# Optimization experiments

Measured on AMD Instinct MI355X. Metric: run time of the kernel, lower is better.

## Reference

```python
import jax, jax.numpy as jnp
import numpy as np

B, T, DIM, HEADS, KPROJ = 4, 4096, 1024, 16, 256
DH = DIM // HEADS  # dim_head = 64


def setup_inputs() -> dict:
    key = jax.random.key(0)
    k1, k2, k3, k4 = jax.random.split(key, 4)
    x = jax.random.normal(k1, (B, T, DIM), dtype=jnp.float32)
    proj_mat = jax.random.normal(k2, (T, KPROJ), dtype=jnp.float32)
    # to_qvk: Linear(dim, 3*dim, bias=False); store as [dim, 3*dim] so y = x @ Wqkv
    Wqkv = jax.random.normal(k3, (DIM, 3 * DIM), dtype=jnp.float32) / np.sqrt(DIM)
    # W_0: Linear(dim, dim, bias=False); stored as [dim, dim] so y = x @ W0
    W0 = jax.random.normal(k4, (DIM, DIM), dtype=jnp.float32) / np.sqrt(DIM)
    return {"x": x, "proj_mat": proj_mat, "Wqkv": Wqkv, "W0": W0}


def reference(x, proj_mat, Wqkv, W0):
    scale = DH ** (-0.5)
    qkv = jnp.einsum('btc,cf->btf', x, Wqkv)  # [B,T,3*dim]
    # einops 'b t (d k h) -> k b h t d' with k=3, h=HEADS: last axis splits as (d, 3, h)
    qkv = qkv.reshape(B, T, DH, 3, HEADS)
    qkv = jnp.transpose(qkv, (3, 0, 4, 1, 2))  # [3, B, H, T, DH]
    q, k, v = qkv[0], qkv[1], qkv[2]
    # Linformer low-rank projection of k and v along sequence axis
    k = jnp.einsum('bhjd,jk->bhkd', k, proj_mat)  # [B,H,KPROJ,DH]
    v = jnp.einsum('bhjd,jk->bhkd', v, proj_mat)
    # scaled dot-product attention
    scores = jnp.einsum('bhid,bhjd->bhij', q, k) * scale  # [B,H,T,KPROJ]
    attn = jax.nn.softmax(scores, axis=-1)
    out = jnp.einsum('bhij,bhjd->bhid', attn, v)  # [B,H,T,DH]
    out = jnp.transpose(out, (0, 2, 1, 3)).reshape(B, T, HEADS * DH)
    return jnp.einsum('btc,cf->btf', out, W0)
```

## Files before the change

### kernel.cpp

```cpp
#include <hip/hip_runtime.h>
#include <stdint.h>
#include <stddef.h>

#define TB    4096
#define NDIM  1024
#define NH    16
#define KPROJ 256
#define DH    64
#define NBH   64

typedef _Float16 f16;
typedef _Float16 f16x8 __attribute__((ext_vector_type(8)));
typedef float    f32x4 __attribute__((ext_vector_type(4)));

__device__ __forceinline__ void glds16(const f16* g, f16* l) {
  __builtin_amdgcn_global_load_lds((const __attribute__((address_space(1))) void*)g,
                                   (__attribute__((address_space(3))) void*)l, 16, 0, 0);
}

__launch_bounds__(256)
__global__ void cvt_x(const float* __restrict__ in, f16* __restrict__ out) {
  size_t i = ((size_t)blockIdx.x * 256 + threadIdx.x) * 8;
  float4 v0 = *(const float4*)(in + i);
  float4 v1 = *(const float4*)(in + i + 4);
  union { f16 h[8]; uint4 u; } pk;
  pk.h[0] = (f16)v0.x; pk.h[1] = (f16)v0.y; pk.h[2] = (f16)v0.z; pk.h[3] = (f16)v0.w;
  pk.h[4] = (f16)v1.x; pk.h[5] = (f16)v1.y; pk.h[6] = (f16)v1.z; pk.h[7] = (f16)v1.w;
  *(uint4*)(out + i) = pk.u;
}

__launch_bounds__(256)
__global__ void cvt_t(const float* __restrict__ in, f16* __restrict__ out, int R, int C) {
  __shared__ __align__(16) f16 s[64][72];
  const int tid = threadIdx.x;
  const int c0 = blockIdx.x * 64, r0 = blockIdx.y * 64;
#pragma unroll
  for (int it = 0; it < 4; ++it) {
    int chunk = it * 256 + tid;
    int r_l = chunk >> 4, c4 = (chunk & 15) * 4;
    float4 v = *(const float4*)(in + (size_t)(r0 + r_l) * C + c0 + c4);
    s[c4 + 0][r_l] = (f16)v.x; s[c4 + 1][r_l] = (f16)v.y;
    s[c4 + 2][r_l] = (f16)v.z; s[c4 + 3][r_l] = (f16)v.w;
  }
  __syncthreads();
#pragma unroll
  for (int it = 0; it < 2; ++it) {
    int chunk = it * 256 + tid;
    int c_l = chunk >> 3, rc = (chunk & 7) * 8;
    *(uint4*)(out + (size_t)(c0 + c_l) * R + r0 + rc) = *(const uint4*)&s[c_l][rc];
  }
}

__launch_bounds__(256)
__global__ void k_qkv(const f16* __restrict__ Xh, const f16* __restrict__ Wt,
                      f16* __restrict__ qt, f16* __restrict__ kvt) {
  __shared__ __align__(16) f16 As[128 * 32];
  __shared__ __align__(16) f16 Bs[128 * 32];
  const int tid = threadIdx.x;
  const int w = tid >> 6, lane = tid & 63;
  const int quad = lane >> 4, l15 = lane & 15;
  const int bn0 = blockIdx.x * 128, bm0 = blockIdx.y * 128;
  const int wm = (w & 1) * 64, wn = (w >> 1) * 64;
  const int srow = lane >> 2, skc = lane & 3;

  f32x4 acc[4][4];
#pragma unroll
  for (int i = 0; i < 4; ++i)
#pragma unroll
    for (int j = 0; j < 4; ++j) acc[i][j] = (f32x4){0.f, 0.f, 0.f, 0.f};

  const f16* Ag0 = Xh + (size_t)(bm0 + w * 32 + srow) * NDIM + skc * 8;
  const f16* Bg0 = Wt + (size_t)(bn0 + w * 32 + srow) * NDIM + skc * 8;
  f16* Al0 = As + (w * 32) * 32;
  f16* Bl0 = Bs + (w * 32) * 32;

  for (int k0 = 0; k0 < NDIM; k0 += 32) {
    glds16(Ag0 + k0, Al0);
    glds16(Ag0 + (size_t)16 * NDIM + k0, Al0 + 16 * 32);
    glds16(Bg0 + k0, Bl0);
    glds16(Bg0 + (size_t)16 * NDIM + k0, Bl0 + 16 * 32);
    __syncthreads();
    f16x8 a[4], b[4];
#pragma unroll
    for (int i = 0; i < 4; ++i) a[i] = *(const f16x8*)(As + (wm + i * 16 + l15) * 32 + quad * 8);
#pragma unroll
    for (int j = 0; j < 4; ++j) b[j] = *(const f16x8*)(Bs + (wn + j * 16 + l15) * 32 + quad * 8);
#pragma unroll
    for (int i = 0; i < 4; ++i)
#pragma unroll
      for (int j = 0; j < 4; ++j)
        acc[i][j] = __builtin_amdgcn_mfma_f32_16x16x32_f16(a[i], b[j], acc[i][j], 0, 0, 0);
    __syncthreads();
  }

#pragma unroll
  for (int i = 0; i < 4; ++i) {
    int mrow = bm0 + wm + i * 16 + quad * 4;
    int bb = mrow >> 12, t = mrow & 4095;
#pragma unroll
    for (int j = 0; j < 4; ++j) {
      int f = bn0 + wn + j * 16 + l15;
      int d = f / 48;
      int rem = f - d * 48;
      int rr = rem >> 4, h = rem & 15;
      f16* base = (rr == 0) ? qt : kvt + (size_t)(rr - 1) * ((size_t)NBH * DH * TB);
      size_t off = ((size_t)((bb * NH + h) * DH + d)) * TB + t;
      union { f16 hh[4]; uint2 u; } pk;
#pragma unroll
      for (int r = 0; r < 4; ++r) pk.hh[r] = (f16)acc[i][j][r];
      *(uint2*)(base + off) = pk.u;
    }
  }
}

__launch_bounds__(256)
__global__ void k_proj(const f16* __restrict__ Pt, const f16* __restrict__ kvt,
                       f16* __restrict__ kpv) {
  __shared__ __align__(16) f16 As[128 * 32];
  __shared__ __align__(16) f16 Bs[64 * 32];
  const int tid = threadIdx.x;
  const int w = tid >> 6, lane = tid & 63;
  const int quad = lane >> 4, l15 = lane & 15;
  const int km0 = blockIdx.x * 128;
  const int bh = blockIdx.y, rv = blockIdx.z;
  const int srow = lane >> 2, skc = lane & 3;
  const f16* Bbase = kvt + (size_t)(rv * NBH + bh) * DH * TB;

  f32x4 acc[2][4];
#pragma unroll
  for (int i = 0; i < 2; ++i)
#pragma unroll
    for (int j = 0; j < 4; ++j) acc[i][j] = (f32x4){0.f, 0.f, 0.f, 0.f};

  const f16* Ag0 = Pt + (size_t)(km0 + w * 32 + srow) * TB + skc * 8;
  const f16* Bg0 = Bbase + (size_t)(w * 16 + srow) * TB + skc * 8;
  f16* Al0 = As + (w * 32) * 32;
  f16* Bl0 = Bs + (w * 16) * 32;

  for (int k0 = 0; k0 < TB; k0 += 32) {
    glds16(Ag0 + k0, Al0);
    glds16(Ag0 + (size_t)16 * TB + k0, Al0 + 16 * 32);
    glds16(Bg0 + k0, Bl0);
    __syncthreads();
    f16x8 a[2], b[4];
#pragma unroll
    for (int i = 0; i < 2; ++i) a[i] = *(const f16x8*)(As + (w * 32 + i * 16 + l15) * 32 + quad * 8);
#pragma unroll
    for (int j = 0; j < 4; ++j) b[j] = *(const f16x8*)(Bs + (j * 16 + l15) * 32 + quad * 8);
#pragma unroll
    for (int i = 0; i < 2; ++i)
#pragma unroll
      for (int j = 0; j < 4; ++j)
        acc[i][j] = __builtin_amdgcn_mfma_f32_16x16x32_f16(a[i], b[j], acc[i][j], 0, 0, 0);
    __syncthreads();
  }

  if (rv == 0) {
#pragma unroll
    for (int i = 0; i < 2; ++i) {
      int kap0 = km0 + w * 32 + i * 16 + quad * 4;
#pragma unroll
      for (int j = 0; j < 4; ++j) {
        int d = j * 16 + l15;
#pragma unroll
        for (int r = 0; r < 4; ++r)
          kpv[((size_t)bh * KPROJ + kap0 + r) * DH + d] = (f16)acc[i][j][r];
      }
    }
  } else {
    f16* vpT = kpv + (size_t)NBH * KPROJ * DH;
#pragma unroll
    for (int i = 0; i < 2; ++i) {
      int kap0 = km0 + w * 32 + i * 16 + quad * 4;
#pragma unroll
      for (int j = 0; j < 4; ++j) {
        int d = j * 16 + l15;
        union { f16 hh[4]; uint2 u; } pk;
#pragma unroll
        for (int r = 0; r < 4; ++r) pk.hh[r] = (f16)acc[i][j][r];
        *(uint2*)&vpT[((size_t)bh * DH + d) * KPROJ + kap0] = pk.u;
      }
    }
  }
}

__launch_bounds__(256)
__global__ void k_attn(const f16* __restrict__ qt, const f16* __restrict__ kpv,
                       f16* __restrict__ aout) {
  __shared__ __align__(16) f16 Ps[4][16][264];
  __shared__ __align__(16) f16 Ks[16384];
  f16* Qs = &Ps[0][0][0];
  const int tid = threadIdx.x;
  const int w = tid >> 6, lane = tid & 63;
  const int quad = lane >> 4, l15 = lane & 15;
  const int bh = blockIdx.y;
  const int tb = blockIdx.x * 64;
  const int b = bh >> 4, h = bh & 15;

  const f16* kpb = kpv + (size_t)bh * (KPROJ * DH);
  const f16* vpb = kpv + (size_t)NBH * KPROJ * DH + (size_t)bh * (DH * KPROJ);

  {
    const f16* qg = qt + (size_t)bh * DH * TB + tb;
#pragma unroll
    for (int c = 0; c < 2; ++c) {
      int d0 = w * 16 + c * 8;
      glds16(qg + (size_t)(d0 + (lane >> 3)) * TB + (lane & 7) * 8, Qs + d0 * 64);
    }
    const int kcolg = ((lane & 7) ^ (lane >> 3)) * 8;
    const int krow0 = w * 64 + (lane >> 3);
#pragma unroll
    for (int it = 0; it < 8; ++it)
      glds16(kpb + (size_t)(krow0 + it * 8) * DH + kcolg, Ks + w * 4096 + it * 512);
  }
  __syncthreads();

  f16x8 aq[2];
#pragma unroll
  for (int ks = 0; ks < 2; ++ks)
#pragma unroll
    for (int j = 0; j < 8; ++j)
      aq[ks][j] = Qs[(ks * 32 + quad * 8 + j) * 64 + w * 16 + l15];

  f32x4 sc[16];
  const int sc0 = (quad ^ (l15 & 7)) * 8;
#pragma unroll
  for (int nt = 0; nt < 16; ++nt) {
    const f16* krow = Ks + (nt * 16 + l15) * 64;
    f16x8 b0 = *(const f16x8*)(krow + sc0);
    f16x8 b1 = *(const f16x8*)(krow + (sc0 ^ 32));
    f32x4 c = (f32x4){0.f, 0.f, 0.f, 0.f};
    c = __builtin_amdgcn_mfma_f32_16x16x32_f16(aq[0], b0, c, 0, 0, 0);
    c = __builtin_amdgcn_mfma_f32_16x16x32_f16(aq[1], b1, c, 0, 0, 0);
    sc[nt] = c;
  }

  float mx[4] = {-1e30f, -1e30f, -1e30f, -1e30f};
#pragma unroll
  for (int nt = 0; nt < 16; ++nt)
#pragma unroll
    for (int r = 0; r < 4; ++r) {
      float s = sc[nt][r] * 0.125f;
      sc[nt][r] = s;
      mx[r] = fmaxf(mx[r], s);
    }
#pragma unroll
  for (int r = 0; r < 4; ++r)
#pragma unroll
    for (int off = 1; off < 16; off <<= 1) mx[r] = fmaxf(mx[r], __shfl_xor(mx[r], off));

  __syncthreads();

  {
#pragma unroll
    for (int it = 0; it < 8; ++it) {
      int r = w * 16 + it * 2 + (lane >> 5);
      int colg = ((lane & 31) ^ (r & 7)) * 8;
      glds16(vpb + (size_t)r * KPROJ + colg, Ks + w * 4096 + it * 512);
    }
  }

  float sm[4] = {0.f, 0.f, 0.f, 0.f};
#pragma unroll
  for (int nt = 0; nt < 16; ++nt)
#pragma unroll
    for (int r = 0; r < 4; ++r) {
      float e = __expf(sc[nt][r] - mx[r]);
      sc[nt][r] = e;
      sm[r] += e;
    }
#pragma unroll
  for (int r = 0; r < 4; ++r)
#pragma unroll
    for (int off = 1; off < 16; off <<= 1) sm[r] += __shfl_xor(sm[r], off);

#pragma unroll
  for (int nt = 0; nt < 16; ++nt)
#pragma unroll
    for (int r = 0; r < 4; ++r) {
      f16 hh = (f16)sc[nt][r];
      uint32_t hb = (uint32_t)__builtin_bit_cast(uint16_t, hh);
      uint32_t nb = (uint32_t)__shfl_xor((int)hb, 1);
      if (!(lane & 1))
        *(uint32_t*)&Ps[w][quad * 4 + r][nt * 16 + l15] = (hb & 0xffffu) | (nb << 16);
    }

  __syncthreads();

  f32x4 oc[4];
#pragma unroll
  for (int j = 0; j < 4; ++j) oc[j] = (f32x4){0.f, 0.f, 0.f, 0.f};
#pragma unroll
  for (int kk = 0; kk < 8; ++kk) {
    f16x8 pa = *(const f16x8*)&Ps[w][l15][kk * 32 + quad * 8];
#pragma unroll
    for (int nd = 0; nd < 4; ++nd) {
      int row = nd * 16 + l15;
      int c = ((kk * 4 + quad) ^ (l15 & 7)) * 8;
      f16x8 bv = *(const f16x8*)(Ks + row * KPROJ + c);
      oc[nd] = __builtin_amdgcn_mfma_f32_16x16x32_f16(pa, bv, oc[nd], 0, 0, 0);
    }
  }

#pragma unroll
  for (int nd = 0; nd < 4; ++nd)
#pragma unroll
    for (int r = 0; r < 4; ++r)
      Ps[w][quad * 4 + r][nd * 16 + l15] = (f16)(oc[nd][r] / sm[r]);

  const int orow = lane >> 3, oc8 = (lane & 7) * 8;
  const size_t obase = ((size_t)b * TB + tb + w * 16) * NDIM + h * 64 + oc8;
#pragma unroll
  for (int g = 0; g < 2; ++g)
    *(f16x8*)(aout + obase + (size_t)(g * 8 + orow) * NDIM) =
        *(const f16x8*)&Ps[w][g * 8 + orow][oc8];
}

__launch_bounds__(256)
__global__ void k_out(const f16* __restrict__ A, const f16* __restrict__ Bt,
                      float* __restrict__ Out) {
  __shared__ __align__(16) f16 As[128 * 32];
  __shared__ __align__(16) f16 Bs[128 * 32];
  const int tid = threadIdx.x;
  const int w = tid >> 6, lane = tid & 63;
  const int quad = lane >> 4, l15 = lane & 15;
  const int bn0 = blockIdx.x * 128, bm0 = blockIdx.y * 128;
  const int wm = (w & 1) * 64, wn = (w >> 1) * 64;
  const int srow = lane >> 2, skc = lane & 3;

  f32x4 acc[4][4];
#pragma unroll
  for (int i = 0; i < 4; ++i)
#pragma unroll
    for (int j = 0; j < 4; ++j) acc[i][j] = (f32x4){0.f, 0.f, 0.f, 0.f};

  const f16* Ag0 = A + (size_t)(bm0 + w * 32 + srow) * NDIM + skc * 8;
  const f16* Bg0 = Bt + (size_t)(bn0 + w * 32 + srow) * NDIM + skc * 8;
  f16* Al0 = As + (w * 32) * 32;
  f16* Bl0 = Bs + (w * 32) * 32;

  for (int k0 = 0; k0 < NDIM; k0 += 32) {
    glds16(Ag0 + k0, Al0);
    glds16(Ag0 + (size_t)16 * NDIM + k0, Al0 + 16 * 32);
    glds16(Bg0 + k0, Bl0);
    glds16(Bg0 + (size_t)16 * NDIM + k0, Bl0 + 16 * 32);
    __syncthreads();
    f16x8 a[4], b[4];
#pragma unroll
    for (int i = 0; i < 4; ++i) a[i] = *(const f16x8*)(As + (wm + i * 16 + l15) * 32 + quad * 8);
#pragma unroll
    for (int j = 0; j < 4; ++j) b[j] = *(const f16x8*)(Bs + (wn + j * 16 + l15) * 32 + quad * 8);
#pragma unroll
    for (int i = 0; i < 4; ++i)
#pragma unroll
      for (int j = 0; j < 4; ++j)
        acc[i][j] = __builtin_amdgcn_mfma_f32_16x16x32_f16(a[i], b[j], acc[i][j], 0, 0, 0);
    __syncthreads();
  }

#pragma unroll
  for (int i = 0; i < 4; ++i) {
    int m = bm0 + wm + i * 16 + quad * 4;
#pragma unroll
    for (int j = 0; j < 4; ++j) {
      int n = bn0 + wn + j * 16 + l15;
#pragma unroll
      for (int r = 0; r < 4; ++r) Out[(size_t)(m + r) * NDIM + n] = acc[i][j][r];
    }
  }
}

extern "C" void kernel_launch(void* const* d_in, const int* in_sizes, int n_in,
                              void* d_out, int out_size, void* d_ws, size_t ws_size,
                              hipStream_t stream) {
  const float* X    = (const float*)d_in[0];
  const float* P    = (const float*)d_in[1];
  const float* Wqkv = (const float*)d_in[2];
  const float* W0   = (const float*)d_in[3];
  float* Out = (float*)d_out;

  char* ws = (char*)d_ws;
  const size_t MB = 1ull << 20;
  f16* Xh   = (f16*)(ws);
  f16* aout = (f16*)(ws);
  f16* qt   = (f16*)(ws + 32 * MB);
  f16* kvt  = (f16*)(ws + 64 * MB);
  f16* kpv  = (f16*)(ws + 128 * MB);
  f16* Wqt  = (f16*)(ws + 132 * MB);
  f16* W0t  = (f16*)(ws + 138 * MB);
  f16* Ptb  = (f16*)(ws + 140 * MB);

  cvt_x<<<dim3(8192), 256, 0, stream>>>(X, Xh);
  cvt_t<<<dim3(48, 16), 256, 0, stream>>>(Wqkv, Wqt, 1024, 3072);
  cvt_t<<<dim3(16, 16), 256, 0, stream>>>(W0, W0t, 1024, 1024);
  cvt_t<<<dim3(4, 64), 256, 0, stream>>>(P, Ptb, 4096, 256);
  k_qkv<<<dim3(24, 128), 256, 0, stream>>>(Xh, Wqt, qt, kvt);
  k_proj<<<dim3(2, 64, 2), 256, 0, stream>>>(Ptb, kvt, kpv);
  k_attn<<<dim3(64, 64), 256, 0, stream>>>(qt, kpv, aout);
  k_out<<<dim3(8, 128), 256, 0, stream>>>(aout, W0t, Out);
}
```

Baseline: 463.8 us.

## Rewrite QKV GEMM with 256x256 tiles, swizzled LDS and pipelined prefetch

The QKV projection kernel moves to 512-thread blocks computing 256x256 output tiles with a k-step of 64. It uses double-buffered LDS slots filled by direct global-to-LDS loads, with explicit vmcnt waits and barriers so loads overlap MFMA work. An XOR swizzle on LDS columns aims to avoid bank conflicts, and setprio raises wave priority during the MFMA bursts. The larger LDS footprint and register count may limit occupancy, and the manual waitcnt scheduling is fragile.

```diff
diff --git a/kernel.cpp b/kernel.cpp
--- a/kernel.cpp
+++ b/kernel.cpp
@@ -51,60 +51,114 @@
   }
 }
 
-__launch_bounds__(256)
+__launch_bounds__(512, 2)
 __global__ void k_qkv(const f16* __restrict__ Xh, const f16* __restrict__ Wt,
                       f16* __restrict__ qt, f16* __restrict__ kvt) {
-  __shared__ __align__(16) f16 As[128 * 32];
-  __shared__ __align__(16) f16 Bs[128 * 32];
+  __shared__ __align__(16) f16 sA[4][128 * 64];
+  __shared__ __align__(16) f16 sB[4][128 * 64];
   const int tid = threadIdx.x;
   const int w = tid >> 6, lane = tid & 63;
   const int quad = lane >> 4, l15 = lane & 15;
-  const int bn0 = blockIdx.x * 128, bm0 = blockIdx.y * 128;
-  const int wm = (w & 1) * 64, wn = (w >> 1) * 64;
-  const int srow = lane >> 2, skc = lane & 3;
-
-  f32x4 acc[4][4];
-#pragma unroll
-  for (int i = 0; i < 4; ++i)
-#pragma unroll
-    for (int j = 0; j < 4; ++j) acc[i][j] = (f32x4){0.f, 0.f, 0.f, 0.f};
-
-  const f16* Ag0 = Xh + (size_t)(bm0 + w * 32 + srow) * NDIM + skc * 8;
-  const f16* Bg0 = Wt + (size_t)(bn0 + w * 32 + srow) * NDIM + skc * 8;
-  f16* Al0 = As + (w * 32) * 32;
-  f16* Bl0 = Bs + (w * 32) * 32;
-
-  for (int k0 = 0; k0 < NDIM; k0 += 32) {
-    glds16(Ag0 + k0, Al0);
-    glds16(Ag0 + (size_t)16 * NDIM + k0, Al0 + 16 * 32);
-    glds16(Bg0 + k0, Bl0);
-    glds16(Bg0 + (size_t)16 * NDIM + k0, Bl0 + 16 * 32);
-    __syncthreads();
-    f16x8 a[4], b[4];
-#pragma unroll
-    for (int i = 0; i < 4; ++i) a[i] = *(const f16x8*)(As + (wm + i * 16 + l15) * 32 + quad * 8);
-#pragma unroll
-    for (int j = 0; j < 4; ++j) b[j] = *(const f16x8*)(Bs + (wn + j * 16 + l15) * 32 + quad * 8);
-#pragma unroll
-    for (int i = 0; i < 4; ++i)
-#pragma unroll
-      for (int j = 0; j < 4; ++j)
-        acc[i][j] = __builtin_amdgcn_mfma_f32_16x16x32_f16(a[i], b[j], acc[i][j], 0, 0, 0);
-    __syncthreads();
-  }
-
-#pragma unroll
-  for (int i = 0; i < 4; ++i) {
-    int mrow = bm0 + wm + i * 16 + quad * 4;
-    int bb = mrow >> 12, t = mrow & 4095;
-#pragma unroll
-    for (int j = 0; j < 4; ++j) {
-      int f = bn0 + wn + j * 16 + l15;
+  const int bn0 = blockIdx.x * 256, bm0 = blockIdx.y * 256;
+
+  const int srow = w * 8 + (lane >> 3);
+  const int scolg = ((lane & 7) ^ (lane >> 3)) * 8;
+  const f16* Ag = Xh + (size_t)(bm0 + srow) * NDIM + scolg;
+  const f16* Bg = Wt + (size_t)(bn0 + srow) * NDIM + scolg;
+
+  auto stage = [&](int H) {
+    int h2 = H & 3, th = H >> 2;
+    int k0 = th * 64;
+    if (h2 < 2) {
+      f16* slot = sB[(th & 1) * 2 + h2];
+      const f16* g = Bg + (size_t)(h2 * 128) * NDIM + k0;
+      glds16(g, slot + w * 512);
+      glds16(g + (size_t)64 * NDIM, slot + 4096 + w * 512);
+    } else {
+      int h = h2 - 2;
+      f16* slot = sA[(th & 1) * 2 + h];
+      const f16* g = Ag + (size_t)(h * 128) * NDIM + k0;
+      glds16(g, slot + w * 512);
+      glds16(g + (size_t)64 * NDIM, slot + 4096 + w * 512);
+    }
+  };
+
+  f32x4 acc[16][2];
+#pragma unroll
+  for (int i = 0; i < 16; ++i)
+#pragma unroll
+    for (int j = 0; j < 2; ++j) acc[i][j] = (f32x4){0.f, 0.f, 0.f, 0.f};
+
+  for (int H = 0; H < 7; ++H) stage(H);
+  asm volatile("s_waitcnt vmcnt(6)" ::: "memory");
+  __builtin_amdgcn_s_barrier();
+  asm volatile("" ::: "memory");
+
+  const int x0 = (quad ^ (l15 & 7)) * 8;
+  const int x1 = x0 ^ 32;
+
+  for (int t = 0; t < 16; ++t) {
+    const f16* aS0 = sA[(t & 1) * 2];
+    const f16* aS1 = sA[(t & 1) * 2 + 1];
+    const f16* bS  = sB[(t & 1) * 2 + (w >> 2)];
+
+    f16x8 bf[2][2];
+#pragma unroll
+    for (int j = 0; j < 2; ++j) {
+      const f16* r = bS + ((w & 3) * 32 + j * 16 + l15) * 64;
+      bf[j][0] = *(const f16x8*)(r + x0);
+      bf[j][1] = *(const f16x8*)(r + x1);
+    }
+
+#pragma unroll
+    for (int q = 0; q < 4; ++q) {
+      const f16* aS = (q >> 1) ? aS1 : aS0;
+      f16x8 af[4][2];
+#pragma unroll
+      for (int i16 = 0; i16 < 4; ++i16) {
+        const f16* r = aS + ((q & 1) * 64 + i16 * 16 + l15) * 64;
+        af[i16][0] = *(const f16x8*)(r + x0);
+        af[i16][1] = *(const f16x8*)(r + x1);
+      }
+      int H = 4 * t + q + 7;
+      if (H < 64) stage(H);
+      asm volatile("" ::: "memory");
+      __builtin_amdgcn_s_barrier();
+      __builtin_amdgcn_s_setprio(1);
+#pragma unroll
+      for (int i16 = 0; i16 < 4; ++i16)
+#pragma unroll
+        for (int j = 0; j < 2; ++j) {
+          acc[q * 4 + i16][j] =
+              __builtin_amdgcn_mfma_f32_16x16x32_f16(af[i16][0], bf[j][0], acc[q * 4 + i16][j], 0, 0, 0);
+          acc[q * 4 + i16][j] =
+              __builtin_amdgcn_mfma_f32_16x16x32_f16(af[i16][1], bf[j][1], acc[q * 4 + i16][j], 0, 0, 0);
+        }
+      __builtin_amdgcn_s_setprio(0);
+      asm volatile("" ::: "memory");
+      __builtin_amdgcn_s_barrier();
+    }
+
+    if (t < 15) {
+      if (t == 14) asm volatile("s_waitcnt vmcnt(0)" ::: "memory");
+      else         asm volatile("s_waitcnt vmcnt(6)" ::: "memory");
+      __builtin_amdgcn_s_barrier();
+      asm volatile("" ::: "memory");
+    }
+  }
+
+#pragma unroll
+  for (int i = 0; i < 16; ++i) {
+    int mrow = bm0 + i * 16 + quad * 4;
+    int bb = mrow >> 12, tt = mrow & 4095;
+#pragma unroll
+    for (int j = 0; j < 2; ++j) {
+      int f = bn0 + w * 32 + j * 16 + l15;
       int d = f / 48;
       int rem = f - d * 48;
       int rr = rem >> 4, h = rem & 15;
       f16* base = (rr == 0) ? qt : kvt + (size_t)(rr - 1) * ((size_t)NBH * DH * TB);
-      size_t off = ((size_t)((bb * NH + h) * DH + d)) * TB + t;
+      size_t off = ((size_t)((bb * NH + h) * DH + d)) * TB + tt;
       union { f16 hh[4]; uint2 u; } pk;
 #pragma unroll
       for (int r = 0; r < 4; ++r) pk.hh[r] = (f16)acc[i][j][r];
@@ -394,7 +448,7 @@
   cvt_t<<<dim3(48, 16), 256, 0, stream>>>(Wqkv, Wqt, 1024, 3072);
   cvt_t<<<dim3(16, 16), 256, 0, stream>>>(W0, W0t, 1024, 1024);
   cvt_t<<<dim3(4, 64), 256, 0, stream>>>(P, Ptb, 4096, 256);
-  k_qkv<<<dim3(24, 128), 256, 0, stream>>>(Xh, Wqt, qt, kvt);
+  k_qkv<<<dim3(12, 64), 512, 0, stream>>>(Xh, Wqt, qt, kvt);
   k_proj<<<dim3(2, 64, 2), 256, 0, stream>>>(Ptb, kvt, kpv);
   k_attn<<<dim3(64, 64), 256, 0, stream>>>(qt, kpv, aout);
   k_out<<<dim3(8, 128), 256, 0, stream>>>(aout, W0t, Out);
```

Result: faster. 448.6 us (-3.3%).

## Reassociate Linformer projection: project X along sequence before K/V weights

Applied to the files above, without the earlier changes.

Instead of computing full K and V for all tokens and then projecting along the sequence, X is first projected by P (Pᵀ·X per batch), then multiplied by the K/V weight slices. The QKV GEMM shrinks to a Q-only GEMM, and the K/V path becomes a small GEMM on the projected rows, removing most of the GEMM FLOPs and the large kvt intermediate. It adds a transposed fp16 copy of X and an extra kernel launch, and changes rounding order (fp16 intermediate Xp).

```diff
diff --git a/kernel.cpp b/kernel.cpp
--- a/kernel.cpp
+++ b/kernel.cpp
@@ -52,8 +52,8 @@
 }
 
 __launch_bounds__(256)
-__global__ void k_qkv(const f16* __restrict__ Xh, const f16* __restrict__ Wt,
-                      f16* __restrict__ qt, f16* __restrict__ kvt) {
+__global__ void k_q(const f16* __restrict__ Xh, const f16* __restrict__ Wt,
+                    f16* __restrict__ qt) {
   __shared__ __align__(16) f16 As[128 * 32];
   __shared__ __align__(16) f16 Bs[128 * 32];
   const int tid = threadIdx.x;
@@ -70,7 +70,9 @@
     for (int j = 0; j < 4; ++j) acc[i][j] = (f32x4){0.f, 0.f, 0.f, 0.f};
 
   const f16* Ag0 = Xh + (size_t)(bm0 + w * 32 + srow) * NDIM + skc * 8;
-  const f16* Bg0 = Wt + (size_t)(bn0 + w * 32 + srow) * NDIM + skc * 8;
+  const int n0 = bn0 + w * 32 + srow, n1 = n0 + 16;
+  const f16* Bg0 = Wt + (size_t)(48 * (n0 & 63) + (n0 >> 6)) * NDIM + skc * 8;
+  const f16* Bg1 = Wt + (size_t)(48 * (n1 & 63) + (n1 >> 6)) * NDIM + skc * 8;
   f16* Al0 = As + (w * 32) * 32;
   f16* Bl0 = Bs + (w * 32) * 32;
 
@@ -78,53 +80,50 @@
     glds16(Ag0 + k0, Al0);
     glds16(Ag0 + (size_t)16 * NDIM + k0, Al0 + 16 * 32);
     glds16(Bg0 + k0, Bl0);
-    glds16(Bg0 + (size_t)16 * NDIM + k0, Bl0 + 16 * 32);
-    __syncthreads();
-    f16x8 a[4], b[4];
+    glds16(Bg1 + k0, Bl0 + 16 * 32);
+    __syncthreads();
+    f16x8 a[4], bfr[4];
 #pragma unroll
     for (int i = 0; i < 4; ++i) a[i] = *(const f16x8*)(As + (wm + i * 16 + l15) * 32 + quad * 8);
 #pragma unroll
-    for (int j = 0; j < 4; ++j) b[j] = *(const f16x8*)(Bs + (wn + j * 16 + l15) * 32 + quad * 8);
+    for (int j = 0; j < 4; ++j) bfr[j] = *(const f16x8*)(Bs + (wn + j * 16 + l15) * 32 + quad * 8);
 #pragma unroll
     for (int i = 0; i < 4; ++i)
 #pragma unroll
       for (int j = 0; j < 4; ++j)
-        acc[i][j] = __builtin_amdgcn_mfma_f32_16x16x32_f16(a[i], b[j], acc[i][j], 0, 0, 0);
+        acc[i][j] = __builtin_amdgcn_mfma_f32_16x16x32_f16(a[i], bfr[j], acc[i][j], 0, 0, 0);
     __syncthreads();
   }
 
 #pragma unroll
   for (int i = 0; i < 4; ++i) {
     int mrow = bm0 + wm + i * 16 + quad * 4;
-    int bb = mrow >> 12, t = mrow & 4095;
+    int bb = mrow >> 12, tt = mrow & 4095;
 #pragma unroll
     for (int j = 0; j < 4; ++j) {
-      int f = bn0 + wn + j * 16 + l15;
-      int d = f / 48;
-      int rem = f - d * 48;
-      int rr = rem >> 4, h = rem & 15;
-      f16* base = (rr == 0) ? qt : kvt + (size_t)(rr - 1) * ((size_t)NBH * DH * TB);
-      size_t off = ((size_t)((bb * NH + h) * DH + d)) * TB + t;
+      int n = bn0 + wn + j * 16 + l15;
+      int h = n >> 6, d = n & 63;
+      size_t off = ((size_t)((bb * NH + h) * DH + d)) * TB + tt;
       union { f16 hh[4]; uint2 u; } pk;
 #pragma unroll
       for (int r = 0; r < 4; ++r) pk.hh[r] = (f16)acc[i][j][r];
-      *(uint2*)(base + off) = pk.u;
-    }
-  }
-}
-
-__launch_bounds__(256)
-__global__ void k_proj(const f16* __restrict__ Pt, const f16* __restrict__ kvt,
-                       f16* __restrict__ kpv) {
+      *(uint2*)(qt + off) = pk.u;
+    }
+  }
+}
+
+__launch_bounds__(256)
+__global__ void k_xp(const f16* __restrict__ Pt, const f16* __restrict__ XhT,
+                     f16* __restrict__ Xp) {
   __shared__ __align__(16) f16 As[128 * 32];
   __shared__ __align__(16) f16 Bs[64 * 32];
   const int tid = threadIdx.x;
   const int w = tid >> 6, lane = tid & 63;
   const int quad = lane >> 4, l15 = lane & 15;
   const int km0 = blockIdx.x * 128;
-  const int bh = blockIdx.y, rv = blockIdx.z;
+  const int c0 = blockIdx.y * 64, b = blockIdx.z;
   const int srow = lane >> 2, skc = lane & 3;
-  const f16* Bbase = kvt + (size_t)(rv * NBH + bh) * DH * TB;
+  const f16* Bbase = XhT + ((size_t)b * NDIM + c0) * TB;
 
   f32x4 acc[2][4];
 #pragma unroll
@@ -142,43 +141,105 @@
     glds16(Ag0 + (size_t)16 * TB + k0, Al0 + 16 * 32);
     glds16(Bg0 + k0, Bl0);
     __syncthreads();
-    f16x8 a[2], b[4];
+    f16x8 a[2], bfr[4];
 #pragma unroll
     for (int i = 0; i < 2; ++i) a[i] = *(const f16x8*)(As + (w * 32 + i * 16 + l15) * 32 + quad * 8);
 #pragma unroll
-    for (int j = 0; j < 4; ++j) b[j] = *(const f16x8*)(Bs + (j * 16 + l15) * 32 + quad * 8);
+    for (int j = 0; j < 4; ++j) bfr[j] = *(const f16x8*)(Bs + (j * 16 + l15) * 32 + quad * 8);
 #pragma unroll
     for (int i = 0; i < 2; ++i)
 #pragma unroll
       for (int j = 0; j < 4; ++j)
-        acc[i][j] = __builtin_amdgcn_mfma_f32_16x16x32_f16(a[i], b[j], acc[i][j], 0, 0, 0);
+        acc[i][j] = __builtin_amdgcn_mfma_f32_16x16x32_f16(a[i], bfr[j], acc[i][j], 0, 0, 0);
+    __syncthreads();
+  }
+
+#pragma unroll
+  for (int i = 0; i < 2; ++i) {
+    int kap0 = km0 + w * 32 + i * 16 + quad * 4;
+#pragma unroll
+    for (int j = 0; j < 4; ++j) {
+      int c = c0 + j * 16 + l15;
+#pragma unroll
+      for (int r = 0; r < 4; ++r)
+        Xp[((size_t)b * KPROJ + kap0 + r) * NDIM + c] = (f16)acc[i][j][r];
+    }
+  }
+}
+
+__launch_bounds__(256)
+__global__ void k_kv(const f16* __restrict__ Xp, const f16* __restrict__ Wt,
+                     f16* __restrict__ kpv) {
+  __shared__ __align__(16) f16 As[128 * 32];
+  __shared__ __align__(16) f16 Bs[128 * 32];
+  const int tid = threadIdx.x;
+  const int w = tid >> 6, lane = tid & 63;
+  const int quad = lane >> 4, l15 = lane & 15;
+  const int bn0 = blockIdx.x * 128, bm0 = blockIdx.y * 128;
+  const int rv = blockIdx.z;
+  const int wm = (w & 1) * 64, wn = (w >> 1) * 64;
+  const int srow = lane >> 2, skc = lane & 3;
+
+  f32x4 acc[4][4];
+#pragma unroll
+  for (int i = 0; i < 4; ++i)
+#pragma unroll
+    for (int j = 0; j < 4; ++j) acc[i][j] = (f32x4){0.f, 0.f, 0.f, 0.f};
+
+  const f16* Ag0 = Xp + (size_t)(bm0 + w * 32 + srow) * NDIM + skc * 8;
+  const int n0 = bn0 + w * 32 + srow, n1 = n0 + 16;
+  const f16* Bg0 = Wt + (size_t)(48 * (n0 & 63) + 16 * (1 + rv) + (n0 >> 6)) * NDIM + skc * 8;
+  const f16* Bg1 = Wt + (size_t)(48 * (n1 & 63) + 16 * (1 + rv) + (n1 >> 6)) * NDIM + skc * 8;
+  f16* Al0 = As + (w * 32) * 32;
+  f16* Bl0 = Bs + (w * 32) * 32;
+
+  for (int k0 = 0; k0 < NDIM; k0 += 32) {
+    glds16(Ag0 + k0, Al0);
+    glds16(Ag0 + (size_t)16 * NDIM + k0, Al0 + 16 * 32);
+    glds16(Bg0 + k0, Bl0);
+    glds16(Bg1 + k0, Bl0 + 16 * 32);
+    __syncthreads();
+    f16x8 a[4], bfr[4];
+#pragma unroll
+    for (int i = 0; i < 4; ++i) a[i] = *(const f16x8*)(As + (wm + i * 16 + l15) * 32 + quad * 8);
+#pragma unroll
+    for (int j = 0; j < 4; ++j) bfr[j] = *(const f16x8*)(Bs + (wn + j * 16 + l15) * 32 + quad * 8);
+#pragma unroll
+    for (int i = 0; i < 4; ++i)
+#pragma unroll
+      for (int j = 0; j < 4; ++j)
+        acc[i][j] = __builtin_amdgcn_mfma_f32_16x16x32_f16(a[i], bfr[j], acc[i][j], 0, 0, 0);
     __syncthreads();
   }
 
   if (rv == 0) {
 #pragma unroll
-    for (int i = 0; i < 2; ++i) {
-      int kap0 = km0 + w * 32 + i * 16 + quad * 4;
+    for (int i = 0; i < 4; ++i) {
+      int m = bm0 + wm + i * 16 + quad * 4;
+      int b = m >> 8, kap = m & 255;
 #pragma unroll
       for (int j = 0; j < 4; ++j) {
-        int d = j * 16 + l15;
+        int n = bn0 + wn + j * 16 + l15;
+        int h = n >> 6, d = n & 63;
 #pragma unroll
         for (int r = 0; r < 4; ++r)
-          kpv[((size_t)bh * KPROJ + kap0 + r) * DH + d] = (f16)acc[i][j][r];
+          kpv[((size_t)(b * NH + h) * KPROJ + kap + r) * DH + d] = (f16)acc[i][j][r];
       }
     }
   } else {
     f16* vpT = kpv + (size_t)NBH * KPROJ * DH;
 #pragma unroll
-    for (int i = 0; i < 2; ++i) {
-      int kap0 = km0 + w * 32 + i * 16 + quad * 4;
+    for (int i = 0; i < 4; ++i) {
+      int m = bm0 + wm + i * 16 + quad * 4;
+      int b = m >> 8, kap = m & 255;
 #pragma unroll
       for (int j = 0; j < 4; ++j) {
-        int d = j * 16 + l15;
+        int n = bn0 + wn + j * 16 + l15;
+        int h = n >> 6, d = n & 63;
         union { f16 hh[4]; uint2 u; } pk;
 #pragma unroll
         for (int r = 0; r < 4; ++r) pk.hh[r] = (f16)acc[i][j][r];
-        *(uint2*)&vpT[((size_t)bh * DH + d) * KPROJ + kap0] = pk.u;
+        *(uint2*)&vpT[((size_t)(b * NH + h) * DH + d) * KPROJ + kap] = pk.u;
       }
     }
   }
@@ -384,7 +445,8 @@
   f16* Xh   = (f16*)(ws);
   f16* aout = (f16*)(ws);
   f16* qt   = (f16*)(ws + 32 * MB);
-  f16* kvt  = (f16*)(ws + 64 * MB);
+  f16* XhT  = (f16*)(ws + 64 * MB);
+  f16* Xp   = (f16*)(ws + 96 * MB);
   f16* kpv  = (f16*)(ws + 128 * MB);
   f16* Wqt  = (f16*)(ws + 132 * MB);
   f16* W0t  = (f16*)(ws + 138 * MB);
@@ -394,8 +456,12 @@
   cvt_t<<<dim3(48, 16), 256, 0, stream>>>(Wqkv, Wqt, 1024, 3072);
   cvt_t<<<dim3(16, 16), 256, 0, stream>>>(W0, W0t, 1024, 1024);
   cvt_t<<<dim3(4, 64), 256, 0, stream>>>(P, Ptb, 4096, 256);
-  k_qkv<<<dim3(24, 128), 256, 0, stream>>>(Xh, Wqt, qt, kvt);
-  k_proj<<<dim3(2, 64, 2), 256, 0, stream>>>(Ptb, kvt, kpv);
+  for (int b = 0; b < 4; ++b)
+    cvt_t<<<dim3(16, 64), 256, 0, stream>>>(X + (size_t)b * 4194304,
+                                            XhT + (size_t)b * 4194304, 4096, 1024);
+  k_q<<<dim3(8, 128), 256, 0, stream>>>(Xh, Wqt, qt);
+  k_xp<<<dim3(2, 16, 4), 256, 0, stream>>>(Ptb, XhT, Xp);
+  k_kv<<<dim3(8, 8, 2), 256, 0, stream>>>(Xp, Wqt, kpv);
   k_attn<<<dim3(64, 64), 256, 0, stream>>>(qt, kpv, aout);
   k_out<<<dim3(8, 128), 256, 0, stream>>>(aout, W0t, Out);
 }
```

Result: faster. 416.5 us (-10.2%).
